# Kernel optimization log

Hardware: AMD Instinct MI355X
Metric: run time of the kernel (lower is better)

## Reference

```python
import jax, jax.numpy as jnp
import numpy as np

DIM = 512
NUM_HEADS = 16
HEAD_DIM = DIM // NUM_HEADS
SCALE = HEAD_DIM ** -0.5  # qk_scale default


def setup_inputs() -> dict:
    key = jax.random.key(0)
    k1, k2, k3 = jax.random.split(key, 3)
    B, nH, nW, C = 8, 256, 49, DIM
    x = jax.random.normal(k1, (B, nH, nW, C), dtype=jnp.float32)
    x_all = jax.random.normal(k2, (B, nH, nW, C), dtype=jnp.float32)
    W_qkv = jax.random.normal(k3, (C, 3 * C), dtype=jnp.float32) * (C ** -0.5)
    b_qkv = jnp.zeros((3 * C,), dtype=jnp.float32)
    return {"x": x, "x_all": x_all, "W_qkv": W_qkv, "b_qkv": b_qkv}


def reference(x, x_all, W_qkv, b_qkv):
    # x: [B, nH, nW, C]  (nH = num windows, nW = tokens per window)
    B, nH, nW, C = x.shape
    qkv = x @ W_qkv + b_qkv                      # [B, nH, nW, 3C]
    qkv = qkv.reshape(B, nH, nW, 3, C)
    q, k, v = qkv[..., 0, :], qkv[..., 1, :], qkv[..., 2, :]
    q = q * SCALE
    attn = jnp.einsum("bwic,bwjc->bwij", q, k)   # [B, nH, nW, nW]
    attn = jax.nn.softmax(attn, axis=-1)
    out = jnp.einsum("bwij,bwjc->bwic", attn, v)  # [B, nH, nW, C]
    return out
```

## Files before the change

kernel.cpp:

```cpp
#include <hip/hip_runtime.h>
#include <stdint.h>

typedef __bf16 bf16;
typedef __bf16 bf16x4 __attribute__((ext_vector_type(4)));
typedef __bf16 bf16x8 __attribute__((ext_vector_type(8)));
typedef float f32x16 __attribute__((ext_vector_type(16)));

#define SCALE 0.17677669529663687f
#define MFMA32(a, b, c) __builtin_amdgcn_mfma_f32_32x32x16_bf16((a), (b), (c), 0, 0, 0)

__device__ __forceinline__ f32x16 fzero16() {
  f32x16 v;
  #pragma unroll
  for (int i = 0; i < 16; ++i) v[i] = 0.f;
  return v;
}

__global__ __launch_bounds__(256) void k_mqk(const float* __restrict__ W, bf16* __restrict__ Mqk) {
  __shared__ float Wkt[32][65];
  __shared__ float Wqt[32][65];
  const int tb = (blockIdx.x >> 4) * 32;
  const int ta = (blockIdx.x & 15) * 32;
  const int tid = threadIdx.x;
  const int a_l = tid & 31, b_l = (tid >> 5) * 4;
  float acc[4] = {0.f, 0.f, 0.f, 0.f};
  for (int c0 = 0; c0 < 512; c0 += 64) {
    __syncthreads();
    for (int i = tid; i < 2048; i += 256) {
      int r = i >> 6, c = i & 63;
      Wkt[r][c] = W[(size_t)(tb + r) * 1536 + 512 + c0 + c];
      Wqt[r][c] = W[(size_t)(ta + r) * 1536 + c0 + c];
    }
    __syncthreads();
    for (int c = 0; c < 64; ++c) {
      float wq = Wqt[a_l][c];
      #pragma unroll
      for (int i = 0; i < 4; ++i) acc[i] += Wkt[b_l + i][c] * wq;
    }
  }
  #pragma unroll
  for (int i = 0; i < 4; ++i)
    Mqk[(size_t)(tb + b_l + i) * 512 + ta + a_l] = (bf16)(SCALE * acc[i]);
}

__global__ __launch_bounds__(256) void k_wvt(const float* __restrict__ W, bf16* __restrict__ WvT) {
  __shared__ float Wt[64][68];
  const int cin0  = (blockIdx.x & 7) * 64;
  const int cout0 = (blockIdx.x >> 3) * 64;
  const int tid = threadIdx.x;
  {
    const int r = tid >> 2, cq = (tid & 3) * 16;
    #pragma unroll
    for (int cc = 0; cc < 4; ++cc) {
      float4 f = *(const float4*)&W[(size_t)(cin0 + r) * 1536 + 1024 + cout0 + cq + 4 * cc];
      Wt[r][cq + 4 * cc + 0] = f.x;
      Wt[r][cq + 4 * cc + 1] = f.y;
      Wt[r][cq + 4 * cc + 2] = f.z;
      Wt[r][cq + 4 * cc + 3] = f.w;
    }
  }
  __syncthreads();
  {
    const int co = tid >> 2, seg = (tid & 3) * 16;
    bf16x8 p0, p1;
    #pragma unroll
    for (int e = 0; e < 8; ++e) p0[e] = (bf16)Wt[seg + e][co];
    #pragma unroll
    for (int e = 0; e < 8; ++e) p1[e] = (bf16)Wt[seg + 8 + e][co];
    *(bf16x8*)&WvT[(size_t)(cout0 + co) * 512 + cin0 + seg]     = p0;
    *(bf16x8*)&WvT[(size_t)(cout0 + co) * 512 + cin0 + seg + 8] = p1;
  }
}

__global__ __launch_bounds__(256) void k_w2(const float* __restrict__ W, const float* __restrict__ bqkv,
                                            float* __restrict__ w2) {
  __shared__ float red[256];
  const int b = blockIdx.x, tid = threadIdx.x;
  float s = W[(size_t)b * 1536 + 512 + tid] * bqkv[tid]
          + W[(size_t)b * 1536 + 512 + 256 + tid] * bqkv[256 + tid];
  red[tid] = s;
  __syncthreads();
  for (int ofs = 128; ofs > 0; ofs >>= 1) {
    if (tid < ofs) red[tid] += red[tid + ofs];
    __syncthreads();
  }
  if (tid == 0) w2[b] = SCALE * red[0];
}

struct SMem {
  bf16 Xs[64][520];
  union { bf16 T1s[64][520]; bf16 Vt[512][72]; } u;
  float Ss[52][65];
  bf16 Ps[64][72];
  float sbias[64];
};

__global__ __launch_bounds__(512, 2) void k_attn(
    const float* __restrict__ x, const float* __restrict__ bqkv,
    const bf16* __restrict__ Mqk, const bf16* __restrict__ WvT,
    const float* __restrict__ w2, float* __restrict__ out) {
  __shared__ SMem sm;
  const int tid = threadIdx.x;
  const int wave = tid >> 6, lane = tid & 63;
  const int lm = lane & 31, hk = lane >> 5;
  const int wid = blockIdx.x;
  const float* xw = x + (size_t)wid * 25088;

  for (int idx = tid; idx < 6272; idx += 512) {
    float4 f = ((const float4*)xw)[idx];
    int row = idx >> 7, c4 = (idx & 127) << 2;
    bf16x4 p;
    p[0] = (bf16)f.x; p[1] = (bf16)f.y; p[2] = (bf16)f.z; p[3] = (bf16)f.w;
    *(bf16x4*)&sm.Xs[row][c4] = p;
  }
  for (int idx = tid; idx < 15 * 130; idx += 512) {
    int r = 49 + idx / 130, c = (idx % 130) * 4;
    bf16x4 z; z[0] = (bf16)0.f; z[1] = (bf16)0.f; z[2] = (bf16)0.f; z[3] = (bf16)0.f;
    *(bf16x4*)&sm.Xs[r][c] = z;
  }
  __syncthreads();

  f32x16 v00, v01, v10, v11;
  {
    const int n_base = wave * 64;
    f32x16 t00 = fzero16(), t01 = fzero16(), t10 = fzero16(), t11 = fzero16();
    v00 = fzero16(); v01 = fzero16(); v10 = fzero16(); v11 = fzero16();
    const bf16* a0p = &sm.Xs[lm][0];
    const bf16* a1p = &sm.Xs[32 + lm][0];
    const bf16* b0g = Mqk + (size_t)(n_base + lm) * 512;
    const bf16* b1g = Mqk + (size_t)(n_base + 32 + lm) * 512;
    const bf16* c0g = WvT + (size_t)(n_base + lm) * 512;
    const bf16* c1g = WvT + (size_t)(n_base + 32 + lm) * 512;
    #pragma unroll 2
    for (int k0 = 0; k0 < 512; k0 += 16) {
      const int ko = k0 + 8 * hk;
      bf16x8 fa0 = *(const bf16x8*)(a0p + ko);
      bf16x8 fa1 = *(const bf16x8*)(a1p + ko);
      bf16x8 fb0 = *(const bf16x8*)(b0g + ko);
      bf16x8 fb1 = *(const bf16x8*)(b1g + ko);
      bf16x8 fc0 = *(const bf16x8*)(c0g + ko);
      bf16x8 fc1 = *(const bf16x8*)(c1g + ko);
      t00 = MFMA32(fa0, fb0, t00); t01 = MFMA32(fa0, fb1, t01);
      t10 = MFMA32(fa1, fb0, t10); t11 = MFMA32(fa1, fb1, t11);
      v00 = MFMA32(fa0, fc0, v00); v01 = MFMA32(fa0, fc1, v01);
      v10 = MFMA32(fa1, fc0, v10); v11 = MFMA32(fa1, fc1, v11);
    }
    #pragma unroll
    for (int reg = 0; reg < 16; ++reg) {
      const int row = (reg & 3) + 8 * (reg >> 2) + 4 * hk;
      sm.u.T1s[row][n_base + lm]           = (bf16)t00[reg];
      sm.u.T1s[row][n_base + 32 + lm]      = (bf16)t01[reg];
      sm.u.T1s[32 + row][n_base + lm]      = (bf16)t10[reg];
      sm.u.T1s[32 + row][n_base + 32 + lm] = (bf16)t11[reg];
    }
  }
  __syncthreads();

  if (wave < 4) {
    const int r = wave & 1, c = wave >> 1;
    f32x16 accS = fzero16();
    const bf16* ap = &sm.u.T1s[32 * r + lm][0];
    const bf16* bp = &sm.Xs[32 * c + lm][0];
    #pragma unroll 4
    for (int k0 = 0; k0 < 512; k0 += 16) {
      const int ko = k0 + 8 * hk;
      bf16x8 fa = *(const bf16x8*)(ap + ko);
      bf16x8 fb = *(const bf16x8*)(bp + ko);
      accS = MFMA32(fa, fb, accS);
    }
    #pragma unroll
    for (int reg = 0; reg < 16; ++reg) {
      const int row = 32 * r + (reg & 3) + 8 * (reg >> 2) + 4 * hk;
      if (row < 52) sm.Ss[row][32 * c + lm] = accS[reg];
    }
  } else {
    const int t2 = tid - 256;
    const int j = t2 >> 2, part = t2 & 3;
    float s = 0.f;
    for (int cc = part * 128; cc < part * 128 + 128; ++cc)
      s += (float)sm.Xs[j][cc] * w2[cc];
    s += __shfl_xor(s, 1);
    s += __shfl_xor(s, 2);
    if (part == 0) sm.sbias[j] = s;
  }
  __syncthreads();

  {
    const int srow = tid >> 3, sub = tid & 7;
    if (srow < 49) {
      float v[8];
      #pragma unroll
      for (int t = 0; t < 8; ++t) {
        const int col = sub + 8 * t;
        v[t] = (col < 49) ? (sm.Ss[srow][col] + sm.sbias[col]) : -1e30f;
      }
      float m = v[0];
      #pragma unroll
      for (int t = 1; t < 8; ++t) m = fmaxf(m, v[t]);
      m = fmaxf(m, __shfl_xor(m, 1, 64));
      m = fmaxf(m, __shfl_xor(m, 2, 64));
      m = fmaxf(m, __shfl_xor(m, 4, 64));
      float e[8]; float ssum = 0.f;
      #pragma unroll
      for (int t = 0; t < 8; ++t) {
        const int col = sub + 8 * t;
        e[t] = (col < 49) ? __expf(v[t] - m) : 0.f;
        ssum += e[t];
      }
      ssum += __shfl_xor(ssum, 1, 64);
      ssum += __shfl_xor(ssum, 2, 64);
      ssum += __shfl_xor(ssum, 4, 64);
      const float inv = 1.f / ssum;
      #pragma unroll
      for (int t = 0; t < 8; ++t)
        sm.Ps[srow][sub + 8 * t] = (bf16)(e[t] * inv);
    }
  }

  {
    const int n_base = wave * 64;
    const float bv0 = bqkv[1024 + n_base + lm];
    const float bv1 = bqkv[1024 + n_base + 32 + lm];
    #pragma unroll
    for (int g = 0; g < 4; ++g) {
      const int t0 = 8 * g + 4 * hk;
      bf16x4 p0, p1, p2, p3;
      #pragma unroll
      for (int j = 0; j < 4; ++j) {
        p0[j] = (bf16)(v00[4 * g + j] + bv0);
        p1[j] = (bf16)(v01[4 * g + j] + bv1);
        p2[j] = (bf16)(v10[4 * g + j] + bv0);
        p3[j] = (bf16)(v11[4 * g + j] + bv1);
      }
      *(bf16x4*)&sm.u.Vt[n_base + lm][t0]           = p0;
      *(bf16x4*)&sm.u.Vt[n_base + 32 + lm][t0]      = p1;
      *(bf16x4*)&sm.u.Vt[n_base + lm][32 + t0]      = p2;
      *(bf16x4*)&sm.u.Vt[n_base + 32 + lm][32 + t0] = p3;
    }
  }
  __syncthreads();

  {
    const int n_base = wave * 64;
    f32x16 a00 = fzero16(), a01 = fzero16(), a10 = fzero16(), a11 = fzero16();
    #pragma unroll
    for (int k0 = 0; k0 < 64; k0 += 16) {
      const int ko = k0 + 8 * hk;
      bf16x8 fa0 = *(const bf16x8*)&sm.Ps[lm][ko];
      bf16x8 fa1 = *(const bf16x8*)&sm.Ps[32 + lm][ko];
      bf16x8 fb0 = *(const bf16x8*)&sm.u.Vt[n_base + lm][ko];
      bf16x8 fb1 = *(const bf16x8*)&sm.u.Vt[n_base + 32 + lm][ko];
      a00 = MFMA32(fa0, fb0, a00); a01 = MFMA32(fa0, fb1, a01);
      a10 = MFMA32(fa1, fb0, a10); a11 = MFMA32(fa1, fb1, a11);
    }
    float* ow = out + (size_t)wid * 25088;
    const int c0_ = n_base + lm, c1_ = n_base + 32 + lm;
    #pragma unroll
    for (int reg = 0; reg < 16; ++reg) {
      const int row = (reg & 3) + 8 * (reg >> 2) + 4 * hk;
      if (row < 49) {
        ow[row * 512 + c0_] = a00[reg];
        ow[row * 512 + c1_] = a01[reg];
      }
      const int row1 = 32 + row;
      if (row1 < 49) {
        ow[row1 * 512 + c0_] = a10[reg];
        ow[row1 * 512 + c1_] = a11[reg];
      }
    }
  }
}

extern "C" void kernel_launch(void* const* d_in, const int* in_sizes, int n_in,
                              void* d_out, int out_size, void* d_ws, size_t ws_size,
                              hipStream_t stream) {
  const float* x    = (const float*)d_in[0];
  const float* W    = (const float*)d_in[2];
  const float* bqkv = (const float*)d_in[3];
  float* out = (float*)d_out;

  bf16*  Mqk = (bf16*)d_ws;
  bf16*  WvT = (bf16*)((char*)d_ws + 512 * 512 * 2);
  float* w2  = (float*)((char*)d_ws + 2 * 512 * 512 * 2);

  k_mqk<<<256, 256, 0, stream>>>(W, Mqk);
  k_wvt<<<64, 256, 0, stream>>>(W, WvT);
  k_w2 <<<512, 256, 0, stream>>>(W, bqkv, w2);
  k_attn<<<2048, 512, 0, stream>>>(x, bqkv, Mqk, WvT, w2, out);
}
```

Measured before the change: 773.3 us.

## Pre-swizzle weight matrices into MFMA fragment order and prefetch B fragments

The setup kernels now write Mqk and WvT in a fragment-major layout, so each lane's 8-element MFMA B operand sits contiguously and a wave's loads are fully coalesced 1KB chunks. The main GEMM loop software-prefetches the next k-step's weight fragments into registers before issuing the current MFMAs, hiding global load latency. The w2 bias dot product now stages w2 in shared memory (aliasing Ps) and uses vectorized bf16x8/float4 loads. This adds register pressure for the prefetched fragments under the two-blocks-per-CU launch bound.

```diff
diff --git a/kernel.cpp b/kernel.cpp
--- a/kernel.cpp
+++ b/kernel.cpp
@@ -16,7 +16,8 @@
   return v;
 }
 
-__global__ __launch_bounds__(256) void k_mqk(const float* __restrict__ W, bf16* __restrict__ Mqk) {
+
+__global__ __launch_bounds__(256) void k_mqk(const float* __restrict__ W, bf16* __restrict__ MqkF) {
   __shared__ float Wkt[32][65];
   __shared__ float Wqt[32][65];
   const int tb = (blockIdx.x >> 4) * 32;
@@ -38,12 +39,17 @@
       for (int i = 0; i < 4; ++i) acc[i] += Wkt[b_l + i][c] * wq;
     }
   }
+  const int col = ta + a_l;
+  const int kc = col >> 4, hkc = (col >> 3) & 1, jc = col & 7;
   #pragma unroll
-  for (int i = 0; i < 4; ++i)
-    Mqk[(size_t)(tb + b_l + i) * 512 + ta + a_l] = (bf16)(SCALE * acc[i]);
-}
-
-__global__ __launch_bounds__(256) void k_wvt(const float* __restrict__ W, bf16* __restrict__ WvT) {
+  for (int i = 0; i < 4; ++i) {
+    const int row = tb + b_l + i;
+    MqkF[(size_t)(((row >> 5) * 32 + kc) * 64 + hkc * 32 + (row & 31)) * 8 + jc]
+        = (bf16)(SCALE * acc[i]);
+  }
+}
+
+__global__ __launch_bounds__(256) void k_wvt(const float* __restrict__ W, bf16* __restrict__ WvTF) {
   __shared__ float Wt[64][68];
   const int cin0  = (blockIdx.x & 7) * 64;
   const int cout0 = (blockIdx.x >> 3) * 64;
@@ -62,13 +68,16 @@
   __syncthreads();
   {
     const int co = tid >> 2, seg = (tid & 3) * 16;
+    const int row = cout0 + co;
     bf16x8 p0, p1;
     #pragma unroll
     for (int e = 0; e < 8; ++e) p0[e] = (bf16)Wt[seg + e][co];
     #pragma unroll
     for (int e = 0; e < 8; ++e) p1[e] = (bf16)Wt[seg + 8 + e][co];
-    *(bf16x8*)&WvT[(size_t)(cout0 + co) * 512 + cin0 + seg]     = p0;
-    *(bf16x8*)&WvT[(size_t)(cout0 + co) * 512 + cin0 + seg + 8] = p1;
+    const size_t base = (size_t)(((row >> 5) * 32 + ((cin0 + seg) >> 4))) * 512
+                      + (size_t)(row & 31) * 8;
+    *(bf16x8*)&WvTF[base]       = p0;
+    *(bf16x8*)&WvTF[base + 256] = p1;
   }
 }
 
@@ -97,9 +106,10 @@
 
 __global__ __launch_bounds__(512, 2) void k_attn(
     const float* __restrict__ x, const float* __restrict__ bqkv,
-    const bf16* __restrict__ Mqk, const bf16* __restrict__ WvT,
+    const bf16* __restrict__ MqkF, const bf16* __restrict__ WvTF,
     const float* __restrict__ w2, float* __restrict__ out) {
   __shared__ SMem sm;
+  float* const ws2 = (float*)&sm.Ps[0][0];
   const int tid = threadIdx.x;
   const int wave = tid >> 6, lane = tid & 63;
   const int lm = lane & 31, hk = lane >> 5;
@@ -118,6 +128,17 @@
     bf16x4 z; z[0] = (bf16)0.f; z[1] = (bf16)0.f; z[2] = (bf16)0.f; z[3] = (bf16)0.f;
     *(bf16x4*)&sm.Xs[r][c] = z;
   }
+  ws2[tid] = w2[tid];
+
+  const size_t lo = (size_t)lane * 8;
+  const bf16* mq0 = MqkF + (size_t)(2 * wave)     * 16384 + lo;
+  const bf16* mq1 = MqkF + (size_t)(2 * wave + 1) * 16384 + lo;
+  const bf16* vv0 = WvTF + (size_t)(2 * wave)     * 16384 + lo;
+  const bf16* vv1 = WvTF + (size_t)(2 * wave + 1) * 16384 + lo;
+  bf16x8 pb0 = *(const bf16x8*)(mq0);
+  bf16x8 pb1 = *(const bf16x8*)(mq1);
+  bf16x8 pc0 = *(const bf16x8*)(vv0);
+  bf16x8 pc1 = *(const bf16x8*)(vv1);
   __syncthreads();
 
   f32x16 v00, v01, v10, v11;
@@ -127,19 +148,19 @@
     v00 = fzero16(); v01 = fzero16(); v10 = fzero16(); v11 = fzero16();
     const bf16* a0p = &sm.Xs[lm][0];
     const bf16* a1p = &sm.Xs[32 + lm][0];
-    const bf16* b0g = Mqk + (size_t)(n_base + lm) * 512;
-    const bf16* b1g = Mqk + (size_t)(n_base + 32 + lm) * 512;
-    const bf16* c0g = WvT + (size_t)(n_base + lm) * 512;
-    const bf16* c1g = WvT + (size_t)(n_base + 32 + lm) * 512;
     #pragma unroll 2
-    for (int k0 = 0; k0 < 512; k0 += 16) {
-      const int ko = k0 + 8 * hk;
+    for (int kc = 0; kc < 32; ++kc) {
+      bf16x8 fb0 = pb0, fb1 = pb1, fc0 = pc0, fc1 = pc1;
+      if (kc + 1 < 32) {
+        const int nx = (kc + 1) * 512;
+        pb0 = *(const bf16x8*)(mq0 + nx);
+        pb1 = *(const bf16x8*)(mq1 + nx);
+        pc0 = *(const bf16x8*)(vv0 + nx);
+        pc1 = *(const bf16x8*)(vv1 + nx);
+      }
+      const int ko = kc * 16 + 8 * hk;
       bf16x8 fa0 = *(const bf16x8*)(a0p + ko);
       bf16x8 fa1 = *(const bf16x8*)(a1p + ko);
-      bf16x8 fb0 = *(const bf16x8*)(b0g + ko);
-      bf16x8 fb1 = *(const bf16x8*)(b1g + ko);
-      bf16x8 fc0 = *(const bf16x8*)(c0g + ko);
-      bf16x8 fc1 = *(const bf16x8*)(c1g + ko);
       t00 = MFMA32(fa0, fb0, t00); t01 = MFMA32(fa0, fb1, t01);
       t10 = MFMA32(fa1, fb0, t10); t11 = MFMA32(fa1, fb1, t11);
       v00 = MFMA32(fa0, fc0, v00); v01 = MFMA32(fa0, fc1, v01);
@@ -176,9 +197,17 @@
   } else {
     const int t2 = tid - 256;
     const int j = t2 >> 2, part = t2 & 3;
+    const bf16* xr = &sm.Xs[j][part * 128];
+    const float* wr = ws2 + part * 128;
     float s = 0.f;
-    for (int cc = part * 128; cc < part * 128 + 128; ++cc)
-      s += (float)sm.Xs[j][cc] * w2[cc];
+    #pragma unroll
+    for (int t = 0; t < 16; ++t) {
+      bf16x8 xv = *(const bf16x8*)(xr + 8 * t);
+      float4 w0 = *(const float4*)(wr + 8 * t);
+      float4 w1 = *(const float4*)(wr + 8 * t + 4);
+      s += (float)xv[0] * w0.x + (float)xv[1] * w0.y + (float)xv[2] * w0.z + (float)xv[3] * w0.w
+         + (float)xv[4] * w1.x + (float)xv[5] * w1.y + (float)xv[6] * w1.z + (float)xv[7] * w1.w;
+    }
     s += __shfl_xor(s, 1);
     s += __shfl_xor(s, 2);
     if (part == 0) sm.sbias[j] = s;
```

Result: faster. 636.7 us (-17.7%).
